# Optimization experiments

Measured on AMD Instinct MI355X. Metric: run time of the kernel, lower is better.

Reference implementation:

```python
import jax, jax.numpy as jnp
import numpy as np

B, CIN, COUT, H, W = 4, 256, 256, 64, 64
K, G = 3, 4
PAD = (K - 1) // 2


def setup_inputs() -> dict:
    key = jax.random.key(0)
    k0, k1, k2, k3 = jax.random.split(key, 4)
    x = jax.random.normal(k0, (B, CIN, H, W), jnp.float32)
    y = jax.random.normal(k1, (B, 2, H, W), jnp.float32)
    # conv_offset: 1x1 conv, no bias, init std=0.1 (normal_init)
    w_offset = jax.random.normal(k2, (G * 2 * K * K, 2, 1, 1), jnp.float32) * 0.1
    # DeformConv2d weight, no bias, init std=0.01
    w_deform = jax.random.normal(k3, (COUT, CIN, K, K), jnp.float32) * 0.01
    return {"x": x, "y": y, "w_offset": w_offset, "w_deform": w_deform}


def _deform_conv(x, offset, weight):
    """DCN v1: stride 1, dilation 1, zero padding PAD, deform_groups=G, groups=1."""
    KK = K * K
    # mmcv offset layout: [B, G*2*KK, H, W] -> per group, per kernel pos, (dy, dx)
    off = offset.reshape(B, G, KK, 2, H, W)
    dy, dx = off[:, :, :, 0], off[:, :, :, 1]            # [B,G,KK,H,W]
    ii, jj = jnp.meshgrid(jnp.arange(K), jnp.arange(K), indexing="ij")
    ky = ii.reshape(KK).astype(x.dtype)                  # kernel row offsets
    kx = jj.reshape(KK).astype(x.dtype)                  # kernel col offsets
    base_y = jnp.arange(H, dtype=x.dtype)[None, :, None] - PAD + ky[:, None, None]  # [KK,H,1]
    base_x = jnp.arange(W, dtype=x.dtype)[None, None, :] - PAD + kx[:, None, None]  # [KK,1,W]
    yc = dy + base_y                                     # [B,G,KK,H,W]
    xc = dx + base_x

    Cg = CIN // G
    xg = x.reshape(B, G, Cg, H, W)

    def sample(xg1, yc1, xc1):
        # xg1 [Cg,H,W]; yc1/xc1 [KK,H,W] -> bilinear sample with zero padding
        y0 = jnp.floor(yc1)
        x0 = jnp.floor(xc1)
        wy = yc1 - y0
        wx = xc1 - x0
        y0i = y0.astype(jnp.int32)
        x0i = x0.astype(jnp.int32)

        def gather(yi, xi):
            valid = (yi >= 0) & (yi < H) & (xi >= 0) & (xi < W)
            v = xg1[:, jnp.clip(yi, 0, H - 1), jnp.clip(xi, 0, W - 1)]  # [Cg,KK,H,W]
            return v * valid[None].astype(xg1.dtype)

        v00 = gather(y0i, x0i)
        v01 = gather(y0i, x0i + 1)
        v10 = gather(y0i + 1, x0i)
        v11 = gather(y0i + 1, x0i + 1)
        return (v00 * (1 - wy) * (1 - wx) + v01 * (1 - wy) * wx
                + v10 * wy * (1 - wx) + v11 * wy * wx)

    sampled = jax.vmap(jax.vmap(sample))(xg, yc, xc)     # [B,G,Cg,KK,H,W]
    sampled = sampled.reshape(B, CIN, KK, H, W)
    wflat = weight.reshape(COUT, CIN, KK)
    return jnp.einsum("bckhw,ock->bohw", sampled, wflat)  # [B,COUT,H,W]


def reference(x, y, w_offset, w_deform):
    # offset = conv_offset(y.detach()), a 1x1 conv without bias
    y_det = jax.lax.stop_gradient(y)
    offset = jnp.einsum("bihw,oi->bohw", y_det, w_offset[:, :, 0, 0])
    out = _deform_conv(x, offset, w_deform)
    return jax.nn.relu(out)
```

## Files before the change

### kernel.cpp

```cpp
#include <hip/hip_runtime.h>
#include <cstddef>

#define B_    4
#define CIN_  256
#define COUT_ 256
#define H_    64
#define W_    64
#define KK_   9
#define G_    4
#define PAD_  1
#define NSL   36

typedef short bf16x8 __attribute__((ext_vector_type(8)));
typedef float f32x4  __attribute__((ext_vector_type(4)));
typedef __attribute__((address_space(1))) const unsigned int* gptr_t;
typedef __attribute__((address_space(3))) unsigned int*       lptr_t;

__device__ __forceinline__ unsigned short f2bf(float v) {
    unsigned int u = __float_as_uint(v);
    u += 0x7fffu + ((u >> 16) & 1u);
    return (unsigned short)(u >> 16);
}
__device__ __forceinline__ float f_lo(unsigned int u) { return __uint_as_float(u << 16); }
__device__ __forceinline__ float f_hi(unsigned int u) { return __uint_as_float(u & 0xffff0000u); }

__global__ __launch_bounds__(256) void prep_kernel(const float* __restrict__ x,
                                                   unsigned short* __restrict__ xT,
                                                   const float* __restrict__ w,
                                                   unsigned short* __restrict__ wb) {
    const int tid = threadIdx.x;
    if (blockIdx.x < 512) {
        __shared__ unsigned short s[128][66];
        const int bh    = blockIdx.x >> 1;
        const int chalf = blockIdx.x & 1;
        const size_t src_base = ((size_t)(bh >> 6) * CIN_ + chalf * 128) * (H_ * W_) + (bh & 63) * W_;
        #pragma unroll 4
        for (int k = 0; k < 32; ++k) {
            int i = k * 256 + tid;
            int c = i >> 6, ww = i & 63;
            s[c][ww] = f2bf(x[src_base + (size_t)c * (H_ * W_) + ww]);
        }
        __syncthreads();
        #pragma unroll 4
        for (int k = 0; k < 16; ++k) {
            int j  = k * 256 + tid;
            int c2 = (j & 63) * 2, ww = j >> 6;
            unsigned int lo = s[c2][ww], hi = s[c2 + 1][ww];
            *(unsigned int*)(xT + ((size_t)bh * 64 + ww) * 256 + chalf * 128 + c2) = lo | (hi << 16);
        }
    } else {
        int idx = (blockIdx.x - 512) * 256 + tid;
        int e   = idx & 7;
        int pos = (idx >> 3) & 7;
        int o   = (idx >> 6) & 255;
        int t   = idx >> 14;
        int g   = t / 9, kk = t - g * 9;
        int j   = pos ^ (o & 7);
        int c   = g * 64 + j * 8 + e;
        wb[idx] = f2bf(w[(o * CIN_ + c) * KK_ + kk]);
    }
}

__global__ __launch_bounds__(512, 2) void dcn_kernel(
    const unsigned short* __restrict__ xT, const float* __restrict__ y,
    const float* __restrict__ w_off, const unsigned short* __restrict__ wb,
    float* __restrict__ out)
{
    __shared__ unsigned short s_W[3][COUT_ * 64];
    __shared__ unsigned short s_S[2][64 * 64];

    const int tid = threadIdx.x;
    const int bid = blockIdx.x;
    const int xcd = bid & 7;
    const int b   = xcd >> 1;
    const int h   = (xcd & 1) * 32 + (bid >> 3);

    const int sp = tid >> 3;
    const int c8 = tid & 7;

    const float yv0 = y[((b * 2 + 0) * H_ + h) * W_ + sp];
    const float yv1 = y[((b * 2 + 1) * H_ + h) * W_ + sp];

    const int lane = tid & 63, wave = tid >> 6;
    const int pg  = wave & 1, oh = wave >> 1;
    const int l15 = lane & 15, kq = lane >> 4, sw = l15 & 7;

    f32x4 acc[8];
    #pragma unroll
    for (int i = 0; i < 8; ++i) acc[i] = (f32x4){0.f, 0.f, 0.f, 0.f};

    const size_t xbase = (size_t)b * (H_ * W_ * 256) + c8 * 8;

    float w00, w01, w10, w11;
    uint4 A, Bv, C, D;

#define ISSUE_SAMPLE(t) do {                                                   \
    const int g_ = (t) / 9, kk_ = (t) % 9;                                     \
    const float4 co = *(const float4*)(w_off + (t) * 4);                       \
    const float dy = fmaf(yv0, co.x, yv1 * co.y);                              \
    const float dx = fmaf(yv0, co.z, yv1 * co.w);                              \
    const float yc = (float)(h + (kk_ / 3) - PAD_) + dy;                       \
    const float xc = (float)(sp + (kk_ % 3) - PAD_) + dx;                      \
    const float yf = floorf(yc), xf = floorf(xc);                              \
    const float wy = yc - yf,    wx = xc - xf;                                 \
    const int   yi = (int)yf,    xi = (int)xf;                                 \
    float a00 = (1.f - wy) * (1.f - wx);                                       \
    float a01 = (1.f - wy) * wx;                                               \
    float a10 = wy * (1.f - wx);                                               \
    float a11 = wy * wx;                                                       \
    const bool y0ok = (yi >= 0) & (yi < H_);                                   \
    const bool y1ok = (yi >= -1) & (yi < H_ - 1);                              \
    const bool x0ok = (xi >= 0) & (xi < W_);                                   \
    const bool x1ok = (xi >= -1) & (xi < W_ - 1);                              \
    w00 = (y0ok & x0ok) ? a00 : 0.f;                                           \
    w01 = (y0ok & x1ok) ? a01 : 0.f;                                           \
    w10 = (y1ok & x0ok) ? a10 : 0.f;                                           \
    w11 = (y1ok & x1ok) ? a11 : 0.f;                                           \
    const int y0c = min(max(yi, 0), H_ - 1);                                   \
    const int y1c = min(max(yi + 1, 0), H_ - 1);                               \
    const int x0c = min(max(xi, 0), W_ - 1);                                   \
    const int x1c = min(max(xi + 1, 0), W_ - 1);                               \
    const unsigned short* xb = xT + xbase + g_ * 64;                           \
    A  = *(const uint4*)(xb + ((size_t)y0c * W_ + x0c) * 256);                 \
    Bv = *(const uint4*)(xb + ((size_t)y0c * W_ + x1c) * 256);                 \
    C  = *(const uint4*)(xb + ((size_t)y1c * W_ + x0c) * 256);                 \
    D  = *(const uint4*)(xb + ((size_t)y1c * W_ + x1c) * 256);                 \
} while (0)

#define STAGE_W(t, buf) do {                                                   \
    const unsigned short* src = wb + (size_t)(t) * 16384;                      \
    _Pragma("unroll")                                                          \
    for (int j = 0; j < 4; ++j) {                                              \
        const int off = (j * 512 + tid) * 8;                                   \
        __builtin_amdgcn_global_load_lds((gptr_t)(src + off),                  \
                                         (lptr_t)(s_W[buf] + off), 16, 0, 0); \
    }                                                                          \
} while (0)

#define WRITE_SAMPLE(buf) do {                                                 \
    const unsigned int av[4] = {A.x, A.y, A.z, A.w};                           \
    const unsigned int bv[4] = {Bv.x, Bv.y, Bv.z, Bv.w};                       \
    const unsigned int cv[4] = {C.x, C.y, C.z, C.w};                           \
    const unsigned int dv[4] = {D.x, D.y, D.z, D.w};                           \
    unsigned int res[4];                                                       \
    _Pragma("unroll")                                                          \
    for (int q = 0; q < 4; ++q) {                                              \
        float rl = w00 * f_lo(av[q]);                                          \
        rl = fmaf(w01, f_lo(bv[q]), rl);                                       \
        rl = fmaf(w10, f_lo(cv[q]), rl);                                       \
        rl = fmaf(w11, f_lo(dv[q]), rl);                                       \
        float rh = w00 * f_hi(av[q]);                                          \
        rh = fmaf(w01, f_hi(bv[q]), rh);                                       \
        rh = fmaf(w10, f_hi(cv[q]), rh);                                       \
        rh = fmaf(w11, f_hi(dv[q]), rh);                                       \
        res[q] = __builtin_amdgcn_perm(__float_as_uint(rh),                    \
                                       __float_as_uint(rl), 0x07060302u);      \
    }                                                                          \
    *(uint4*)(s_S[buf] + sp * 64 + ((c8 ^ (sp & 7)) * 8)) =                    \
        make_uint4(res[0], res[1], res[2], res[3]);                            \
} while (0)

#define MFMA_STEP(wb_, sb_) do {                                               \
    bf16x8 bf[2][2], af[2][4];                                                 \
    _Pragma("unroll")                                                          \
    for (int kh = 0; kh < 2; ++kh) {                                           \
        const int pos = ((kh * 4 + kq) ^ sw) * 8;                              \
        _Pragma("unroll")                                                      \
        for (int nt = 0; nt < 2; ++nt)                                         \
            bf[kh][nt] = *(const bf16x8*)(s_S[sb_] +                           \
                              (pg * 32 + nt * 16 + l15) * 64 + pos);           \
        _Pragma("unroll")                                                      \
        for (int mt = 0; mt < 4; ++mt)                                         \
            af[kh][mt] = *(const bf16x8*)(s_W[wb_] +                           \
                              (oh * 64 + mt * 16 + l15) * 64 + pos);           \
    }                                                                          \
    __builtin_amdgcn_s_setprio(1);                                             \
    _Pragma("unroll")                                                          \
    for (int kh = 0; kh < 2; ++kh)                                             \
        _Pragma("unroll")                                                      \
        for (int nt = 0; nt < 2; ++nt)                                         \
            _Pragma("unroll")                                                  \
            for (int mt = 0; mt < 4; ++mt)                                     \
                acc[nt * 4 + mt] = __builtin_amdgcn_mfma_f32_16x16x32_bf16(    \
                    af[kh][mt], bf[kh][nt], acc[nt * 4 + mt], 0, 0, 0);        \
    __builtin_amdgcn_s_setprio(0);                                             \
} while (0)

#define STEP(s_, WCUR, WPRE, SCUR, SNXT, DO_ISS, DO_STG, DO_BAR) do {          \
    if (DO_ISS) ISSUE_SAMPLE((s_) + 1);                                        \
    __builtin_amdgcn_sched_barrier(0);                                         \
    if (DO_STG) STAGE_W((s_) + 2, WPRE);                                       \
    __builtin_amdgcn_sched_barrier(0);                                         \
    MFMA_STEP(WCUR, SCUR);                                                     \
    __builtin_amdgcn_sched_barrier(0);                                         \
    if (DO_ISS) WRITE_SAMPLE(SNXT);                                            \
    __builtin_amdgcn_sched_barrier(0);                                         \
    if (DO_BAR) {                                                              \
        asm volatile("s_waitcnt lgkmcnt(0)" ::: "memory");                     \
        __builtin_amdgcn_sched_barrier(0);                                     \
        __builtin_amdgcn_s_barrier();                                          \
        __builtin_amdgcn_sched_barrier(0);                                     \
    }                                                                          \
} while (0)

    ISSUE_SAMPLE(0);
    __builtin_amdgcn_sched_barrier(0);
    STAGE_W(0, 0);
    __builtin_amdgcn_sched_barrier(0);
    WRITE_SAMPLE(0);
    __builtin_amdgcn_sched_barrier(0);
    STAGE_W(1, 1);
    __builtin_amdgcn_sched_barrier(0);
    asm volatile("s_waitcnt vmcnt(4) lgkmcnt(0)" ::: "memory");
    __builtin_amdgcn_sched_barrier(0);
    __builtin_amdgcn_s_barrier();
    __builtin_amdgcn_sched_barrier(0);

    for (int sb = 0; sb < 30; sb += 6) {
        STEP(sb + 0, 0, 2, 0, 1, 1, 1, 1);
        STEP(sb + 1, 1, 0, 1, 0, 1, 1, 1);
        STEP(sb + 2, 2, 1, 0, 1, 1, 1, 1);
        STEP(sb + 3, 0, 2, 1, 0, 1, 1, 1);
        STEP(sb + 4, 1, 0, 0, 1, 1, 1, 1);
        STEP(sb + 5, 2, 1, 1, 0, 1, 1, 1);
    }
    STEP(30, 0, 2, 0, 1, 1, 1, 1);
    STEP(31, 1, 0, 1, 0, 1, 1, 1);
    STEP(32, 2, 1, 0, 1, 1, 1, 1);
    STEP(33, 0, 2, 1, 0, 1, 1, 1);
    STEP(34, 1, 0, 0, 1, 1, 0, 1);
    STEP(35, 2, 1, 1, 0, 0, 0, 0);

    #pragma unroll
    for (int nt = 0; nt < 2; ++nt) {
        const int px = pg * 32 + nt * 16 + l15;
        #pragma unroll
        for (int mt = 0; mt < 4; ++mt) {
            const int obase = oh * 64 + mt * 16 + kq * 4;
            #pragma unroll
            for (int r = 0; r < 4; ++r) {
                out[(((size_t)b * COUT_ + obase + r) * H_ + h) * W_ + px] =
                    fmaxf(acc[nt * 4 + mt][r], 0.f);
            }
        }
    }
#undef ISSUE_SAMPLE
#undef STAGE_W
#undef WRITE_SAMPLE
#undef MFMA_STEP
#undef STEP
}

extern "C" void kernel_launch(void* const* d_in, const int* in_sizes, int n_in,
                              void* d_out, int out_size, void* d_ws, size_t ws_size,
                              hipStream_t stream) {
    const float* x     = (const float*)d_in[0];
    const float* y     = (const float*)d_in[1];
    const float* w_off = (const float*)d_in[2];
    const float* w_def = (const float*)d_in[3];
    float* out = (float*)d_out;

    unsigned short* xT = (unsigned short*)d_ws;
    unsigned short* wb = (unsigned short*)d_ws + 4194304;

    prep_kernel<<<2816, 256, 0, stream>>>(x, xT, w_def, wb);
    dcn_kernel<<<256, 512, 0, stream>>>(xT, y, w_off, wb, out);
}
```

Measured before the change: 121.5 us.

## Split output channels across two blocks of 256 threads per row

Each block now computes half of the output channels (128) for one (batch,row), which doubles the grid to 512 blocks of 256 threads and halves the weight LDS buffers. Each thread samples two 8-channel chunks instead of one, so the bilinear sampling work is duplicated across the two channel-half blocks. The intent is better occupancy and more blocks to fill the CUs, paid for with redundant gathers and interpolation.

```diff
diff --git a/kernel.cpp b/kernel.cpp
--- a/kernel.cpp
+++ b/kernel.cpp
@@ -61,22 +61,24 @@
     }
 }
 
-__global__ __launch_bounds__(512, 2) void dcn_kernel(
+__global__ __launch_bounds__(256, 4) void dcn_kernel(
     const unsigned short* __restrict__ xT, const float* __restrict__ y,
     const float* __restrict__ w_off, const unsigned short* __restrict__ wb,
     float* __restrict__ out)
 {
-    __shared__ unsigned short s_W[3][COUT_ * 64];
+    __shared__ unsigned short s_W[3][128 * 64];
     __shared__ unsigned short s_S[2][64 * 64];
 
     const int tid = threadIdx.x;
     const int bid = blockIdx.x;
-    const int xcd = bid & 7;
-    const int b   = xcd >> 1;
-    const int h   = (xcd & 1) * 32 + (bid >> 3);
-
-    const int sp = tid >> 3;
-    const int c8 = tid & 7;
+    const int ohalf = bid >> 8;
+    const int r     = bid & 255;
+    const int xcd   = r & 7;
+    const int b     = xcd >> 1;
+    const int h     = (xcd & 1) * 32 + (r >> 3);
+
+    const int sp = tid >> 2;
+    const int cq = (tid & 3) * 2;
 
     const float yv0 = y[((b * 2 + 0) * H_ + h) * W_ + sp];
     const float yv1 = y[((b * 2 + 1) * H_ + h) * W_ + sp];
@@ -89,10 +91,10 @@
     #pragma unroll
     for (int i = 0; i < 8; ++i) acc[i] = (f32x4){0.f, 0.f, 0.f, 0.f};
 
-    const size_t xbase = (size_t)b * (H_ * W_ * 256) + c8 * 8;
+    const size_t xbase = (size_t)b * (H_ * W_ * 256) + cq * 8;
 
     float w00, w01, w10, w11;
-    uint4 A, Bv, C, D;
+    uint4 A0, B0, C0, D0, A1, B1, C1, D1;
 
 #define ISSUE_SAMPLE(t) do {                                                   \
     const int g_ = (t) / 9, kk_ = (t) % 9;                                     \
@@ -121,28 +123,31 @@
     const int x0c = min(max(xi, 0), W_ - 1);                                   \
     const int x1c = min(max(xi + 1, 0), W_ - 1);                               \
     const unsigned short* xb = xT + xbase + g_ * 64;                           \
-    A  = *(const uint4*)(xb + ((size_t)y0c * W_ + x0c) * 256);                 \
-    Bv = *(const uint4*)(xb + ((size_t)y0c * W_ + x1c) * 256);                 \
-    C  = *(const uint4*)(xb + ((size_t)y1c * W_ + x0c) * 256);                 \
-    D  = *(const uint4*)(xb + ((size_t)y1c * W_ + x1c) * 256);                 \
+    const unsigned short* p00 = xb + ((size_t)y0c * W_ + x0c) * 256;           \
+    const unsigned short* p01 = xb + ((size_t)y0c * W_ + x1c) * 256;           \
+    const unsigned short* p10 = xb + ((size_t)y1c * W_ + x0c) * 256;           \
+    const unsigned short* p11 = xb + ((size_t)y1c * W_ + x1c) * 256;           \
+    A0 = *(const uint4*)(p00);      A1 = *(const uint4*)(p00 + 8);             \
+    B0 = *(const uint4*)(p01);      B1 = *(const uint4*)(p01 + 8);             \
+    C0 = *(const uint4*)(p10);      C1 = *(const uint4*)(p10 + 8);             \
+    D0 = *(const uint4*)(p11);      D1 = *(const uint4*)(p11 + 8);             \
 } while (0)
 
 #define STAGE_W(t, buf) do {                                                   \
-    const unsigned short* src = wb + (size_t)(t) * 16384;                      \
+    const unsigned short* src = wb + (size_t)(t) * 16384 + ohalf * 8192;       \
     _Pragma("unroll")                                                          \
     for (int j = 0; j < 4; ++j) {                                              \
-        const int off = (j * 512 + tid) * 8;                                   \
+        const int off = (j * 256 + tid) * 8;                                   \
         __builtin_amdgcn_global_load_lds((gptr_t)(src + off),                  \
                                          (lptr_t)(s_W[buf] + off), 16, 0, 0); \
     }                                                                          \
 } while (0)
 
-#define WRITE_SAMPLE(buf) do {                                                 \
-    const unsigned int av[4] = {A.x, A.y, A.z, A.w};                           \
-    const unsigned int bv[4] = {Bv.x, Bv.y, Bv.z, Bv.w};                       \
-    const unsigned int cv[4] = {C.x, C.y, C.z, C.w};                           \
-    const unsigned int dv[4] = {D.x, D.y, D.z, D.w};                           \
-    unsigned int res[4];                                                       \
+#define BILIN(Aq, Bq, Cq, Dq, res) do {                                        \
+    const unsigned int av[4] = {Aq.x, Aq.y, Aq.z, Aq.w};                       \
+    const unsigned int bv[4] = {Bq.x, Bq.y, Bq.z, Bq.w};                       \
+    const unsigned int cv[4] = {Cq.x, Cq.y, Cq.z, Cq.w};                       \
+    const unsigned int dv[4] = {Dq.x, Dq.y, Dq.z, Dq.w};                       \
     _Pragma("unroll")                                                          \
     for (int q = 0; q < 4; ++q) {                                              \
         float rl = w00 * f_lo(av[q]);                                          \
@@ -156,8 +161,16 @@
         res[q] = __builtin_amdgcn_perm(__float_as_uint(rh),                    \
                                        __float_as_uint(rl), 0x07060302u);      \
     }                                                                          \
-    *(uint4*)(s_S[buf] + sp * 64 + ((c8 ^ (sp & 7)) * 8)) =                    \
-        make_uint4(res[0], res[1], res[2], res[3]);                            \
+} while (0)
+
+#define WRITE_SAMPLE(buf) do {                                                 \
+    unsigned int res0[4], res1[4];                                             \
+    BILIN(A0, B0, C0, D0, res0);                                               \
+    BILIN(A1, B1, C1, D1, res1);                                               \
+    *(uint4*)(s_S[buf] + sp * 64 + (((cq + 0) ^ (sp & 7)) * 8)) =              \
+        make_uint4(res0[0], res0[1], res0[2], res0[3]);                        \
+    *(uint4*)(s_S[buf] + sp * 64 + (((cq + 1) ^ (sp & 7)) * 8)) =              \
+        make_uint4(res1[0], res1[1], res1[2], res1[3]);                        \
 } while (0)
 
 #define MFMA_STEP(wb_, sb_) do {                                               \
@@ -236,16 +249,17 @@
         const int px = pg * 32 + nt * 16 + l15;
         #pragma unroll
         for (int mt = 0; mt < 4; ++mt) {
-            const int obase = oh * 64 + mt * 16 + kq * 4;
+            const int obase = ohalf * 128 + oh * 64 + mt * 16 + kq * 4;
             #pragma unroll
-            for (int r = 0; r < 4; ++r) {
-                out[(((size_t)b * COUT_ + obase + r) * H_ + h) * W_ + px] =
-                    fmaxf(acc[nt * 4 + mt][r], 0.f);
+            for (int rr = 0; rr < 4; ++rr) {
+                out[(((size_t)b * COUT_ + obase + rr) * H_ + h) * W_ + px] =
+                    fmaxf(acc[nt * 4 + mt][rr], 0.f);
             }
         }
     }
 #undef ISSUE_SAMPLE
 #undef STAGE_W
+#undef BILIN
 #undef WRITE_SAMPLE
 #undef MFMA_STEP
 #undef STEP
@@ -264,5 +278,5 @@
     unsigned short* wb = (unsigned short*)d_ws + 4194304;
 
     prep_kernel<<<2816, 256, 0, stream>>>(x, xT, w_def, wb);
-    dcn_kernel<<<256, 512, 0, stream>>>(xT, y, w_off, wb, out);
-}
+    dcn_kernel<<<512, 256, 0, stream>>>(xT, y, w_off, wb, out);
+}
```

Result: slower. 124.0 us (+2.1%).
